# Kernel tuning notes

Hardware: AMD Instinct MI355X
Metric: run time of the kernel (lower is better)

## Reference

```python
import jax, jax.numpy as jnp
import numpy as np

B, N, D = 32, 2048, 1024


def setup_inputs() -> dict:
    key0 = jax.random.key(0)
    ks = jax.random.split(key0, 9)
    scale = 1.0 / np.sqrt(D)
    query = jax.random.normal(ks[0], (B, D), dtype=jnp.float32)
    key = jax.random.normal(ks[1], (B, N, D), dtype=jnp.float32)
    mask = jax.random.randint(ks[2], (B, N), 0, 2, dtype=jnp.int32)
    W1 = jax.random.uniform(ks[3], (D, D), jnp.float32, -scale, scale)
    b1 = jax.random.uniform(ks[4], (D,), jnp.float32, -scale, scale)
    W2 = jax.random.uniform(ks[5], (D, D), jnp.float32, -scale, scale)
    b2 = jax.random.uniform(ks[6], (D,), jnp.float32, -scale, scale)
    v_w = jax.random.uniform(ks[7], (D,), jnp.float32, -scale, scale)
    v_b = jax.random.uniform(ks[8], (), jnp.float32, -scale, scale)
    return {"query": query, "key": key, "mask": mask,
            "W1": W1, "b1": b1, "W2": W2, "b2": b2, "v_w": v_w, "v_b": v_b}


def reference(query, key, mask, W1, b1, W2, b2, v_w, v_b):
    # key_out: [B, N, D] = key @ W1^T + b1 (nn.Linear convention)
    key_out = jnp.einsum('bnd,ed->bne', key, W1) + b1
    # query_out: [B, D] -> broadcast over N
    query_out = jnp.einsum('bd,ed->be', query, W2) + b2
    h = jnp.tanh(key_out + query_out[:, None, :])  # [B, N, D]
    ui = jnp.einsum('bnd,d->bn', h, v_w) + v_b      # v: D -> 1, squeezed
    ui = jnp.where(mask.astype(bool), ui, -jnp.inf)
    return ui
```

## Files before the change

### kernel.cpp

```cpp
#include <hip/hip_runtime.h>
#include <hip/hip_bf16.h>
#include <math.h>

#define B_ 32
#define N_ 2048
#define D_ 1024
#define M_ (B_ * N_)

typedef float  fx4  __attribute__((ext_vector_type(4)));
typedef float  fx2  __attribute__((ext_vector_type(2)));
typedef __bf16 bf16x8 __attribute__((ext_vector_type(8)));
typedef unsigned short us4 __attribute__((ext_vector_type(4)));

#define WS_T 2097152ULL

#define MASK_NEG_SENTINEL (-1.0e30f)

__device__ inline unsigned short f2b(float f) {
    __hip_bfloat16 h = __float2bfloat16(f);
    return *reinterpret_cast<unsigned short*>(&h);
}

__global__ void w1_convert_kernel(const fx4* __restrict__ W1,
                                  us4* __restrict__ w1b4) {
    int idx = blockIdx.x * blockDim.x + threadIdx.x;
#pragma unroll
    for (int i = 0; i < 4; ++i) {
        int j = idx + i * 65536;
        fx4 v = W1[j];
        us4 o; o.x = f2b(v.x); o.y = f2b(v.y); o.z = f2b(v.z); o.w = f2b(v.w);
        w1b4[j] = o;
    }
}

__global__ void tq_kernel(const float* __restrict__ query,
                          const float* __restrict__ W2,
                          const float* __restrict__ b1,
                          const float* __restrict__ b2,
                          float* __restrict__ t) {
    int tid = threadIdx.x;
    int p = blockIdx.x * 32 + (tid >> 3);
    int j = tid & 7;
    int b = p >> 10;
    int e = p & 1023;
    const fx4* q = (const fx4*)query + (size_t)b * 256;
    const fx4* w = (const fx4*)W2 + (size_t)e * 256;
    float acc = 0.f;
#pragma unroll 4
    for (int it = 0; it < 32; ++it) {
        int k4 = it * 8 + j;
        fx4 qv = q[k4];
        fx4 wv = w[k4];
        acc += qv.x * wv.x + qv.y * wv.y + qv.z * wv.z + qv.w * wv.w;
    }
    acc += __shfl_xor(acc, 1);
    acc += __shfl_xor(acc, 2);
    acc += __shfl_xor(acc, 4);
    if (j == 0) t[p] = acc + b1[e] + b2[e];
}

__device__ inline float fast_tanh(float x) {
    float ax = fabsf(x);
    float e  = __expf(-2.0f * ax);
    float r  = (1.0f - e) / (1.0f + e);
    return copysignf(r, x);
}

#define BM 64
#define BK 32

#define GLD16(g, l)                                                        \
    __builtin_amdgcn_global_load_lds(                                      \
        (const __attribute__((address_space(1))) void*)(g),                \
        (__attribute__((address_space(3))) void*)(l), 16, 0, 0)

__global__ void __launch_bounds__(1024, 4)
fused_main(const float* __restrict__ key,
           const unsigned short* __restrict__ w1b,
           const float* __restrict__ t,
           const float* __restrict__ v_w,
           const float* __restrict__ v_b,
           const int* __restrict__ mask,
           float* __restrict__ out) {
    __shared__ unsigned short Bs0[D_ * BK];
    __shared__ unsigned short Bs1[D_ * BK];
    __shared__ unsigned short As0[BM * BK];
    __shared__ unsigned short As1[BM * BK];
    __shared__ float rs[16][BM];

    const int tid  = threadIdx.x;
    const int lane = tid & 63;
    const int wave = tid >> 6;
    const int quad = lane >> 4;
    const int l15  = lane & 15;
    const int m0   = blockIdx.x * BM;

    const int sB  = (lane & 7) ^ (lane >> 3);
    const int eL  = ((lane >> 3) << 1) | (sB >> 2);
    const int ksB = sB & 3;
    const unsigned short* bsrc =
        w1b + (size_t)(wave * 64 + eL) * D_ + ksB * 8;

    const int arow = tid >> 4;
    const int akk  = tid & 15;
    const float* asrc = key + (size_t)(m0 + arow) * D_ + akk * 2;
    const int aP  = arow >> 1;
    const int asl = (((arow & 1) << 2) | (akk >> 2)) ^ (aP & 7);
    const int aDstOff = aP * 128 + asl * 16 + (akk & 3) * 4;

    int aOff[4], bOff[4];
#pragma unroll
    for (int i = 0; i < 4; ++i) {
        int row = i * 16 + l15;
        aOff[i] = (row >> 1) * 128 +
                  ((((row & 1) << 2) | quad) ^ ((row >> 1) & 7)) * 16;
    }
#pragma unroll
    for (int j = 0; j < 4; ++j) {
        int e = wave * 64 + j * 16 + l15;
        bOff[j] = (e >> 1) * 128 +
                  ((((e & 1) << 2) | quad) ^ ((e >> 1) & 7)) * 16;
    }

    fx4 acc[4][4] = {};
    fx2 aNext;

    {
        char* bd = (char*)Bs0 + wave * 4096;
#pragma unroll
        for (int q = 0; q < 4; ++q)
            GLD16(bsrc + q * 16 * D_, bd + q * 1024);
        fx2 v0 = *(const fx2*)asrc;
        aNext   = *(const fx2*)(asrc + BK);
        unsigned int pk = f2b(v0.x) | ((unsigned int)f2b(v0.y) << 16);
        *(unsigned int*)((char*)As0 + aDstOff) = pk;
        asm volatile("s_waitcnt lgkmcnt(0)" ::: "memory");
        __builtin_amdgcn_s_barrier();
        asm volatile("" ::: "memory");
    }

#pragma unroll 2
    for (int tt = 0; tt < 30; ++tt) {
        const int p = tt & 1;
        const unsigned short* BsP = p ? Bs1 : Bs0;
        unsigned short*       BsQ = p ? Bs0 : Bs1;
        const unsigned short* AsP = p ? As1 : As0;
        unsigned short*       AsQ = p ? As0 : As1;

        char* bd = (char*)BsQ + wave * 4096;
#pragma unroll
        for (int q = 0; q < 4; ++q)
            GLD16(bsrc + q * 16 * D_ + (size_t)(tt + 1) * BK, bd + q * 1024);
        fx2 aFut = *(const fx2*)(asrc + (size_t)(tt + 2) * BK);
        unsigned int pk = f2b(aNext.x) | ((unsigned int)f2b(aNext.y) << 16);
        *(unsigned int*)((char*)AsQ + aDstOff) = pk;
        asm volatile("s_waitcnt vmcnt(6)" ::: "memory");
        bf16x8 a[4], b[4];
#pragma unroll
        for (int i = 0; i < 4; ++i)
            a[i] = *(const bf16x8*)((const char*)AsP + aOff[i]);
#pragma unroll
        for (int j = 0; j < 4; ++j)
            b[j] = *(const bf16x8*)((const char*)BsP + bOff[j]);
        __builtin_amdgcn_s_setprio(1);
#pragma unroll
        for (int i = 0; i < 4; ++i)
#pragma unroll
            for (int j = 0; j < 4; ++j)
                acc[i][j] = __builtin_amdgcn_mfma_f32_16x16x32_bf16(
                    a[i], b[j], acc[i][j], 0, 0, 0);
        __builtin_amdgcn_s_setprio(0);
        aNext = aFut;
        asm volatile("s_waitcnt lgkmcnt(0)" ::: "memory");
        __builtin_amdgcn_s_barrier();
        asm volatile("" ::: "memory");
    }

    {
        char* bd = (char*)Bs1 + wave * 4096;
#pragma unroll
        for (int q = 0; q < 4; ++q)
            GLD16(bsrc + q * 16 * D_ + (size_t)31 * BK, bd + q * 1024);
        unsigned int pk = f2b(aNext.x) | ((unsigned int)f2b(aNext.y) << 16);
        *(unsigned int*)((char*)As1 + aDstOff) = pk;
        asm volatile("s_waitcnt vmcnt(4)" ::: "memory");
        bf16x8 a[4], b[4];
#pragma unroll
        for (int i = 0; i < 4; ++i)
            a[i] = *(const bf16x8*)((const char*)As0 + aOff[i]);
#pragma unroll
        for (int j = 0; j < 4; ++j)
            b[j] = *(const bf16x8*)((const char*)Bs0 + bOff[j]);
        __builtin_amdgcn_s_setprio(1);
#pragma unroll
        for (int i = 0; i < 4; ++i)
#pragma unroll
            for (int j = 0; j < 4; ++j)
                acc[i][j] = __builtin_amdgcn_mfma_f32_16x16x32_bf16(
                    a[i], b[j], acc[i][j], 0, 0, 0);
        __builtin_amdgcn_s_setprio(0);
        asm volatile("s_waitcnt lgkmcnt(0)" ::: "memory");
        __builtin_amdgcn_s_barrier();
        asm volatile("" ::: "memory");
    }
    {
        asm volatile("s_waitcnt vmcnt(0)" ::: "memory");
        __builtin_amdgcn_sched_barrier(0);
        bf16x8 a[4], b[4];
#pragma unroll
        for (int i = 0; i < 4; ++i)
            a[i] = *(const bf16x8*)((const char*)As1 + aOff[i]);
#pragma unroll
        for (int j = 0; j < 4; ++j)
            b[j] = *(const bf16x8*)((const char*)Bs1 + bOff[j]);
#pragma unroll
        for (int i = 0; i < 4; ++i)
#pragma unroll
            for (int j = 0; j < 4; ++j)
                acc[i][j] = __builtin_amdgcn_mfma_f32_16x16x32_bf16(
                    a[i], b[j], acc[i][j], 0, 0, 0);
    }

    const float* trow = t + (size_t)(m0 >> 11) * D_;
    float vwv[4], tqv[4];
#pragma unroll
    for (int j = 0; j < 4; ++j) {
        int e = wave * 64 + j * 16 + l15;
        vwv[j] = v_w[e];
        tqv[j] = trow[e];
    }
#pragma unroll
    for (int i = 0; i < 4; ++i)
#pragma unroll
        for (int r = 0; r < 4; ++r) {
            float s = 0.f;
#pragma unroll
            for (int j = 0; j < 4; ++j)
                s += vwv[j] * fast_tanh(acc[i][j][r] + tqv[j]);
            s += __shfl_xor(s, 1);
            s += __shfl_xor(s, 2);
            s += __shfl_xor(s, 4);
            s += __shfl_xor(s, 8);
            if (l15 == 0) rs[wave][i * 16 + quad * 4 + r] = s;
        }
    __syncthreads();

    if (tid < BM) {
        float u = 0.f;
#pragma unroll
        for (int w = 0; w < 16; ++w) u += rs[w][tid];
        const int m = m0 + tid;
        out[m] = mask[m] ? (u + v_b[0]) : MASK_NEG_SENTINEL;
    }
}

extern "C" void kernel_launch(void* const* d_in, const int* in_sizes, int n_in,
                              void* d_out, int out_size, void* d_ws, size_t ws_size,
                              hipStream_t stream) {
    const float* query = (const float*)d_in[0];
    const float* key   = (const float*)d_in[1];
    const int*   mask  = (const int*)d_in[2];
    const float* W1    = (const float*)d_in[3];
    const float* b1    = (const float*)d_in[4];
    const float* W2    = (const float*)d_in[5];
    const float* b2    = (const float*)d_in[6];
    const float* v_w   = (const float*)d_in[7];
    const float* v_b   = (const float*)d_in[8];

    char* ws = (char*)d_ws;
    unsigned short* w1b = (unsigned short*)ws;
    float*          t   = (float*)(ws + WS_T);

    w1_convert_kernel<<<256, 256, 0, stream>>>((const fx4*)W1, (us4*)w1b);
    tq_kernel<<<1024, 256, 0, stream>>>(query, W2, b1, b2, t);
    fused_main<<<M_ / BM, 1024, 0, stream>>>(key, w1b, t, v_w, v_b, mask,
                                             (float*)d_out);
}
```

Baseline: 600.3 us.

## Load W1 tiles directly into registers instead of staging through LDS

Removes the double-buffered LDS staging of the bf16 W1 tiles (global_load_lds plus ds_read) and has each wave load its B fragments straight from global memory into registers, double-buffered across k-steps. The A (key) prefetch now runs two steps ahead. This frees about 128KB of LDS and cuts LDS traffic for B. In exchange, every block reads W1 straight from global memory, which raises L2 traffic and register pressure, and the explicit vmcnt waits are gone, leaving load ordering to the compiler.

```diff
diff --git a/kernel.cpp b/kernel.cpp
--- a/kernel.cpp
+++ b/kernel.cpp
@@ -69,11 +69,6 @@
 #define BM 64
 #define BK 32
 
-#define GLD16(g, l)                                                        \
-    __builtin_amdgcn_global_load_lds(                                      \
-        (const __attribute__((address_space(1))) void*)(g),                \
-        (__attribute__((address_space(3))) void*)(l), 16, 0, 0)
-
 __global__ void __launch_bounds__(1024, 4)
 fused_main(const float* __restrict__ key,
            const unsigned short* __restrict__ w1b,
@@ -82,8 +77,6 @@
            const float* __restrict__ v_b,
            const int* __restrict__ mask,
            float* __restrict__ out) {
-    __shared__ unsigned short Bs0[D_ * BK];
-    __shared__ unsigned short Bs1[D_ * BK];
     __shared__ unsigned short As0[BM * BK];
     __shared__ unsigned short As1[BM * BK];
     __shared__ float rs[16][BM];
@@ -95,11 +88,15 @@
     const int l15  = lane & 15;
     const int m0   = blockIdx.x * BM;
 
-    const int sB  = (lane & 7) ^ (lane >> 3);
-    const int eL  = ((lane >> 3) << 1) | (sB >> 2);
-    const int ksB = sB & 3;
-    const unsigned short* bsrc =
-        w1b + (size_t)(wave * 64 + eL) * D_ + ksB * 8;
+    const unsigned short* bbase =
+        w1b + (size_t)(wave * 64 + l15) * D_ + quad * 8;
+
+#define LOADB(dst, kk)                                                     \
+    do {                                                                   \
+        _Pragma("unroll")                                                  \
+        for (int j_ = 0; j_ < 4; ++j_)                                     \
+            dst[j_] = *(const bf16x8*)(bbase + (size_t)j_ * 16 * D_ + (kk)); \
+    } while (0)
 
     const int arow = tid >> 4;
     const int akk  = tid & 15;
@@ -108,30 +105,24 @@
     const int asl = (((arow & 1) << 2) | (akk >> 2)) ^ (aP & 7);
     const int aDstOff = aP * 128 + asl * 16 + (akk & 3) * 4;
 
-    int aOff[4], bOff[4];
+    int aOff[4];
 #pragma unroll
     for (int i = 0; i < 4; ++i) {
         int row = i * 16 + l15;
         aOff[i] = (row >> 1) * 128 +
                   ((((row & 1) << 2) | quad) ^ ((row >> 1) & 7)) * 16;
     }
-#pragma unroll
-    for (int j = 0; j < 4; ++j) {
-        int e = wave * 64 + j * 16 + l15;
-        bOff[j] = (e >> 1) * 128 +
-                  ((((e & 1) << 2) | quad) ^ ((e >> 1) & 7)) * 16;
-    }
 
     fx4 acc[4][4] = {};
-    fx2 aNext;
+    bf16x8 b0[4], b1[4];
+    fx2 aN1, aN2;
 
     {
-        char* bd = (char*)Bs0 + wave * 4096;
-#pragma unroll
-        for (int q = 0; q < 4; ++q)
-            GLD16(bsrc + q * 16 * D_, bd + q * 1024);
+        LOADB(b0, 0);
+        LOADB(b1, BK);
         fx2 v0 = *(const fx2*)asrc;
-        aNext   = *(const fx2*)(asrc + BK);
+        aN1 = *(const fx2*)(asrc + BK);
+        aN2 = *(const fx2*)(asrc + 2 * BK);
         unsigned int pk = f2b(v0.x) | ((unsigned int)f2b(v0.y) << 16);
         *(unsigned int*)((char*)As0 + aDstOff) = pk;
         asm volatile("s_waitcnt lgkmcnt(0)" ::: "memory");
@@ -142,83 +133,76 @@
 #pragma unroll 2
     for (int tt = 0; tt < 30; ++tt) {
         const int p = tt & 1;
-        const unsigned short* BsP = p ? Bs1 : Bs0;
-        unsigned short*       BsQ = p ? Bs0 : Bs1;
         const unsigned short* AsP = p ? As1 : As0;
         unsigned short*       AsQ = p ? As0 : As1;
 
-        char* bd = (char*)BsQ + wave * 4096;
-#pragma unroll
-        for (int q = 0; q < 4; ++q)
-            GLD16(bsrc + q * 16 * D_ + (size_t)(tt + 1) * BK, bd + q * 1024);
-        fx2 aFut = *(const fx2*)(asrc + (size_t)(tt + 2) * BK);
-        unsigned int pk = f2b(aNext.x) | ((unsigned int)f2b(aNext.y) << 16);
+        unsigned int pk = f2b(aN1.x) | ((unsigned int)f2b(aN1.y) << 16);
         *(unsigned int*)((char*)AsQ + aDstOff) = pk;
-        asm volatile("s_waitcnt vmcnt(6)" ::: "memory");
-        bf16x8 a[4], b[4];
+        aN1 = aN2;
+        int ka = tt + 3; if (ka > 31) ka = 31;
+        aN2 = *(const fx2*)(asrc + (size_t)ka * BK);
+
+        bf16x8 a[4];
 #pragma unroll
         for (int i = 0; i < 4; ++i)
             a[i] = *(const bf16x8*)((const char*)AsP + aOff[i]);
-#pragma unroll
-        for (int j = 0; j < 4; ++j)
-            b[j] = *(const bf16x8*)((const char*)BsP + bOff[j]);
+
         __builtin_amdgcn_s_setprio(1);
-#pragma unroll
-        for (int i = 0; i < 4; ++i)
-#pragma unroll
-            for (int j = 0; j < 4; ++j)
-                acc[i][j] = __builtin_amdgcn_mfma_f32_16x16x32_bf16(
-                    a[i], b[j], acc[i][j], 0, 0, 0);
+        if (p == 0) {
+#pragma unroll
+            for (int i = 0; i < 4; ++i)
+#pragma unroll
+                for (int j = 0; j < 4; ++j)
+                    acc[i][j] = __builtin_amdgcn_mfma_f32_16x16x32_bf16(
+                        a[i], b0[j], acc[i][j], 0, 0, 0);
+        } else {
+#pragma unroll
+            for (int i = 0; i < 4; ++i)
+#pragma unroll
+                for (int j = 0; j < 4; ++j)
+                    acc[i][j] = __builtin_amdgcn_mfma_f32_16x16x32_bf16(
+                        a[i], b1[j], acc[i][j], 0, 0, 0);
+        }
         __builtin_amdgcn_s_setprio(0);
-        aNext = aFut;
+
+        if (p == 0) { LOADB(b0, (size_t)(tt + 2) * BK); }
+        else        { LOADB(b1, (size_t)(tt + 2) * BK); }
+
         asm volatile("s_waitcnt lgkmcnt(0)" ::: "memory");
         __builtin_amdgcn_s_barrier();
         asm volatile("" ::: "memory");
     }
 
     {
-        char* bd = (char*)Bs1 + wave * 4096;
-#pragma unroll
-        for (int q = 0; q < 4; ++q)
-            GLD16(bsrc + q * 16 * D_ + (size_t)31 * BK, bd + q * 1024);
-        unsigned int pk = f2b(aNext.x) | ((unsigned int)f2b(aNext.y) << 16);
+        unsigned int pk = f2b(aN1.x) | ((unsigned int)f2b(aN1.y) << 16);
         *(unsigned int*)((char*)As1 + aDstOff) = pk;
-        asm volatile("s_waitcnt vmcnt(4)" ::: "memory");
-        bf16x8 a[4], b[4];
+        bf16x8 a[4];
 #pragma unroll
         for (int i = 0; i < 4; ++i)
             a[i] = *(const bf16x8*)((const char*)As0 + aOff[i]);
-#pragma unroll
-        for (int j = 0; j < 4; ++j)
-            b[j] = *(const bf16x8*)((const char*)Bs0 + bOff[j]);
         __builtin_amdgcn_s_setprio(1);
 #pragma unroll
         for (int i = 0; i < 4; ++i)
 #pragma unroll
             for (int j = 0; j < 4; ++j)
                 acc[i][j] = __builtin_amdgcn_mfma_f32_16x16x32_bf16(
-                    a[i], b[j], acc[i][j], 0, 0, 0);
+                    a[i], b0[j], acc[i][j], 0, 0, 0);
         __builtin_amdgcn_s_setprio(0);
         asm volatile("s_waitcnt lgkmcnt(0)" ::: "memory");
         __builtin_amdgcn_s_barrier();
         asm volatile("" ::: "memory");
     }
     {
-        asm volatile("s_waitcnt vmcnt(0)" ::: "memory");
-        __builtin_amdgcn_sched_barrier(0);
-        bf16x8 a[4], b[4];
+        bf16x8 a[4];
 #pragma unroll
         for (int i = 0; i < 4; ++i)
             a[i] = *(const bf16x8*)((const char*)As1 + aOff[i]);
-#pragma unroll
-        for (int j = 0; j < 4; ++j)
-            b[j] = *(const bf16x8*)((const char*)Bs1 + bOff[j]);
 #pragma unroll
         for (int i = 0; i < 4; ++i)
 #pragma unroll
             for (int j = 0; j < 4; ++j)
                 acc[i][j] = __builtin_amdgcn_mfma_f32_16x16x32_bf16(
-                    a[i], b[j], acc[i][j], 0, 0, 0);
+                    a[i], b1[j], acc[i][j], 0, 0, 0);
     }
 
     const float* trow = t + (size_t)(m0 >> 11) * D_;
```

Measured after the change: 746.3 us. 24.3% more time.
